# Optimization experiments

Hardware: AMD Instinct MI355X
Metric: run time of the kernel (lower is better)

Reference implementation:

```python
import jax, jax.numpy as jnp
import numpy as np

B, S, N, P = 16, 1, 6, 70000
H0, W0, DS = 448, 800, 4
H, W = H0 // DS, W0 // DS          # 112, 200
BEV_SIDE = 200


def _apply_4x4(RT, xyz):
    # RT: [M,4,4], xyz: [M,P,3] -> [M,P,3]
    xyz1 = jnp.concatenate([xyz, jnp.ones_like(xyz[..., :1])], axis=-1)
    return jnp.einsum('mij,mpj->mpi', RT, xyz1)[..., :3]


def _scale_intrinsics4(K, sx, sy):
    # K: [M,3,3] pinhole intrinsics -> scaled, embedded in 4x4
    M = K.shape[0]
    K4 = jnp.tile(jnp.eye(4, dtype=K.dtype), (M, 1, 1))
    K4 = K4.at[:, 0, 0].set(K[:, 0, 0] * sx)
    K4 = K4.at[:, 1, 1].set(K[:, 1, 1] * sy)
    K4 = K4.at[:, 0, 2].set(K[:, 0, 2] * sx)
    K4 = K4.at[:, 1, 2].set(K[:, 1, 2] * sy)
    return K4


def setup_inputs() -> dict:
    rng = np.random.default_rng(0)
    pts = rng.uniform(-50.0, 50.0, size=(B, 1, 1, P, 3)).astype(np.float32)
    pts[..., 2] = rng.uniform(-2.0, 4.0, size=(B, 1, 1, P)).astype(np.float32)
    ilu = rng.uniform(0.0, 255.0, size=(B, 1, 1, P, 1)).astype(np.float32)
    pcloud = np.concatenate([pts, ilu], axis=-1)
    # extrinsics: cam-to-car pose, 6 cameras at yaw 0..300deg
    E = np.tile(np.eye(4, dtype=np.float32), (B, S, N, 1, 1))
    for n in range(N):
        a = 2.0 * np.pi * n / N
        c, s = np.cos(a), np.sin(a)
        E[:, :, n, :3, :3] = np.array([[c, -s, 0], [s, c, 0], [0, 0, 1]], np.float32)
        E[:, :, n, :3, 3] = np.array([2.0 * c, 2.0 * s, 1.5], np.float32)
    K = np.tile(np.eye(3, dtype=np.float32), (B, S, N, 1, 1))
    K[..., 0, 0] = 500.0
    K[..., 1, 1] = 500.0
    K[..., 0, 2] = W0 / 2.0
    K[..., 1, 2] = H0 / 2.0
    V = np.tile(np.eye(4, dtype=np.float32), (B, 1, 1, 1, 1))
    V[..., 0, 0] = 2.0
    V[..., 1, 1] = 2.0
    V[..., 0, 3] = 100.0
    V[..., 1, 3] = 100.0
    return {
        'pcloud': jnp.asarray(pcloud),
        'extrinsics': jnp.asarray(E),
        'intrinsics': jnp.asarray(K),
        'view': jnp.asarray(V),
        'bev_side': BEV_SIDE,
    }


def reference(pcloud, extrinsics, intrinsics, view, bev_side):
    sx = sy = 1.0 / DS
    bsn = B * S * N
    lidar_coords = pcloud[:, 0, 0, :, :3]                      # [B,P,3]
    ilu = jnp.repeat(pcloud[:, 0, 0, :, 3], N, axis=0)         # [BSN,P]
    view2 = view[:, 0, 0]                                      # [B,4,4]
    lidar_view = _apply_4x4(jnp.linalg.inv(view2), lidar_coords)
    xyz_car = jnp.repeat(lidar_view, N, axis=0)                # [BSN,P,3]
    K = intrinsics.reshape(bsn, 3, 3)
    E = extrinsics.reshape(bsn, 4, 4)
    Rt = jnp.swapaxes(E[:, :3, :3], 1, 2)
    Einv = E.at[:, :3, :3].set(Rt).at[:, :3, 3:4].set(-jnp.matmul(Rt, E[:, :3, 3:4]))
    pixel_from_car = jnp.matmul(_scale_intrinsics4(K, sx, sy), Einv)
    z = _apply_4x4(Einv, xyz_car)[:, :, 2]                     # cam-frame depth
    xyz_pixel = _apply_4x4(pixel_from_car, xyz_car)            # [BSN,P,3]
    normalizer = xyz_pixel[:, :, 2]
    xy = xyz_pixel[:, :, :2] / jnp.maximum(normalizer[..., None], 1e-6)
    x_, y_ = xy[:, :, 0], xy[:, :, 1]
    valid = ((x_ > -0.5) & (x_ < W - 0.5) & (y_ > -0.5) & (y_ < H - 0.5) & (z > 0.0)).astype(pcloud.dtype)
    depth = jnp.clip(normalizer, 0.0, bev_side / 2 - 1) * valid
    vilu = jnp.clip(ilu * valid, 0.0, 255.0)
    ym = jnp.clip(y_, 0.0, H - 1).astype(jnp.int32)
    xm = jnp.clip(x_, 0.0, W - 1).astype(jnp.int32)
    b = jnp.broadcast_to(jnp.arange(bsn)[:, None], (bsn, P))
    depth_grid = jnp.zeros((bsn, H, W), pcloud.dtype).at[b, ym, xm].set(depth)
    ilu_grid = jnp.zeros((bsn, H, W), pcloud.dtype).at[b, ym, xm].set(vilu)
    ilu_grid = jnp.log1p(ilu_grid) / np.log(256.0)
    depth_grid = depth_grid / (bev_side / 2)
    return jnp.concatenate([depth_grid[:, None], ilu_grid[:, None]], axis=1)  # [BSN,2,H,W]
```

## Files before the change

kernel.cpp:

```cpp
#include <hip/hip_runtime.h>
#include <math.h>

#define B_    16
#define N_    6
#define P_    70000
#define H_    112
#define W_    200
#define HW_   (H_ * W_)
#define BSN_  (B_ * N_)
#define QROWS  28
#define QCELLS (QROWS * W_)
#define NSLAB  4
#define THREADS_ 1024

#define NBUCKET (BSN_ * NSLAB)
#define ARENA_U32 ((size_t)NBUCKET * P_)
#define WS_NEED ((ARENA_U32 + 2 * NBUCKET) * 4)

#define CC0 0
#define CC1 199
#define CC2 28416
#define CC3 28615


__device__ __forceinline__ float rdot(const float r[4], float x, float y, float z) {
    float s = r[0] * x;
    s = fmaf(r[1], y, s);
    s = fmaf(r[2], z, s);
    return s + r[3];
}

__device__ __forceinline__ float rdot4(float r0, float r1, float r2, float r3,
                                       float x, float y, float z) {
    float s = r0 * x;
    s = fmaf(r1, y, s);
    s = fmaf(r2, z, s);
    return s + r3;
}

__device__ __forceinline__ void inv4(const float* m, float* o) {
    float inv[16];
    inv[0]  =  m[5]*m[10]*m[15] - m[5]*m[11]*m[14] - m[9]*m[6]*m[15] + m[9]*m[7]*m[14] + m[13]*m[6]*m[11] - m[13]*m[7]*m[10];
    inv[4]  = -m[4]*m[10]*m[15] + m[4]*m[11]*m[14] + m[8]*m[6]*m[15] - m[8]*m[7]*m[14] - m[12]*m[6]*m[11] + m[12]*m[7]*m[10];
    inv[8]  =  m[4]*m[9]*m[15]  - m[4]*m[11]*m[13] - m[8]*m[5]*m[15] + m[8]*m[7]*m[13] + m[12]*m[5]*m[11] - m[12]*m[7]*m[9];
    inv[12] = -m[4]*m[9]*m[14]  + m[4]*m[10]*m[13] + m[8]*m[5]*m[14] - m[8]*m[6]*m[13] - m[12]*m[5]*m[10] + m[12]*m[6]*m[9];
    inv[1]  = -m[1]*m[10]*m[15] + m[1]*m[11]*m[14] + m[9]*m[2]*m[15] - m[9]*m[3]*m[14] - m[13]*m[2]*m[11] + m[13]*m[3]*m[10];
    inv[5]  =  m[0]*m[10]*m[15] - m[0]*m[11]*m[14] - m[8]*m[2]*m[15] + m[8]*m[3]*m[14] + m[12]*m[2]*m[11] - m[12]*m[3]*m[10];
    inv[9]  = -m[0]*m[9]*m[15]  + m[0]*m[11]*m[13] + m[8]*m[1]*m[15] - m[8]*m[3]*m[13] - m[12]*m[1]*m[11] + m[12]*m[3]*m[9];
    inv[13] =  m[0]*m[9]*m[14]  - m[0]*m[10]*m[13] - m[8]*m[1]*m[14] + m[8]*m[2]*m[13] + m[12]*m[1]*m[10] - m[12]*m[2]*m[9];
    inv[2]  =  m[1]*m[6]*m[15]  - m[1]*m[7]*m[14]  - m[5]*m[2]*m[15] + m[5]*m[3]*m[14] + m[13]*m[2]*m[7]  - m[13]*m[3]*m[6];
    inv[6]  = -m[0]*m[6]*m[15]  + m[0]*m[7]*m[14]  + m[4]*m[2]*m[15] - m[4]*m[3]*m[14] - m[12]*m[2]*m[7]  + m[12]*m[3]*m[6];
    inv[10] =  m[0]*m[5]*m[15]  - m[0]*m[7]*m[13]  - m[4]*m[1]*m[15] + m[4]*m[3]*m[13] + m[12]*m[1]*m[7]  - m[12]*m[3]*m[5];
    inv[14] = -m[0]*m[5]*m[14]  + m[0]*m[6]*m[13]  + m[4]*m[1]*m[14] - m[4]*m[2]*m[13] - m[12]*m[1]*m[6]  + m[12]*m[2]*m[5];
    inv[3]  = -m[1]*m[6]*m[11]  + m[1]*m[7]*m[10]  + m[5]*m[2]*m[11] - m[5]*m[3]*m[10] - m[9]*m[2]*m[7]   + m[9]*m[3]*m[6];
    inv[7]  =  m[0]*m[6]*m[11]  - m[0]*m[7]*m[10]  - m[4]*m[2]*m[11] + m[4]*m[3]*m[10] + m[8]*m[2]*m[7]   - m[8]*m[3]*m[6];
    inv[11] = -m[0]*m[5]*m[11]  + m[0]*m[7]*m[9]   + m[4]*m[1]*m[11] - m[4]*m[3]*m[9]  - m[8]*m[1]*m[7]   + m[8]*m[3]*m[5];
    inv[15] =  m[0]*m[5]*m[10]  - m[0]*m[6]*m[9]   - m[4]*m[1]*m[10] + m[4]*m[2]*m[9]  + m[8]*m[1]*m[6]   - m[8]*m[2]*m[5];
    float det = m[0]*inv[0] + m[1]*inv[4] + m[2]*inv[8] + m[3]*inv[12];
    float rdet = 1.0f / det;
    for (int i = 0; i < 16; ++i) o[i] = inv[i] * rdet;
}

__device__ __forceinline__ void cam_mats(const float* Ein, const float* Kin,
                                         float E2[4], float PFC[3][4]) {
    float Einv[4][4];
    for (int i = 0; i < 3; ++i)
        for (int j = 0; j < 3; ++j)
            Einv[i][j] = Ein[j * 4 + i];
    for (int i = 0; i < 3; ++i) {
        float s = Ein[0 * 4 + i] * Ein[0 * 4 + 3];
        s = fmaf(Ein[1 * 4 + i], Ein[1 * 4 + 3], s);
        s = fmaf(Ein[2 * 4 + i], Ein[2 * 4 + 3], s);
        Einv[i][3] = -s;
    }
    Einv[3][0] = Ein[12]; Einv[3][1] = Ein[13];
    Einv[3][2] = Ein[14]; Einv[3][3] = Ein[15];

    float K4[4][4] = {};
    K4[0][0] = Kin[0] * 0.25f;  K4[0][2] = Kin[2] * 0.25f;
    K4[1][1] = Kin[4] * 0.25f;  K4[1][2] = Kin[5] * 0.25f;
    K4[2][2] = 1.0f;            K4[3][3] = 1.0f;

    for (int i = 0; i < 3; ++i)
        for (int j = 0; j < 4; ++j) {
            float s = K4[i][0] * Einv[0][j];
            s = fmaf(K4[i][1], Einv[1][j], s);
            s = fmaf(K4[i][2], Einv[2][j], s);
            s = fmaf(K4[i][3], Einv[3][j], s);
            PFC[i][j] = s;
        }
    for (int j = 0; j < 4; ++j) E2[j] = Einv[2][j];
}


__global__ __launch_bounds__(2 * NBUCKET) void k_init_meta(int* __restrict__ meta) {
    const int t = threadIdx.x;
    meta[t] = (t < NBUCKET) ? 0 : -1;
}


#define K1CH 69

__global__ __launch_bounds__(THREADS_) void k_bucket2(
        const float4* __restrict__ pc, const float* __restrict__ extr,
        const float* __restrict__ intr, const float* __restrict__ view,
        unsigned int* __restrict__ arena, int* __restrict__ cursors,
        int* __restrict__ gcorner) {
    __shared__ float sM[84];
    __shared__ int   cnt[16][24];
    __shared__ int   wbase[16][24];
    __shared__ int   gb[24];
    __shared__ int   lc[24];

    const int b    = blockIdx.x;
    const int t    = threadIdx.x;
    const int lane = t & 63;
    const int w    = t >> 6;

    if (t == 0) {
        float Vi[16];
        inv4(&view[b * 16], Vi);
        for (int k = 0; k < 12; ++k) sM[k] = Vi[k];
    } else if (t >= 64 && t < 64 + N_) {
        int n = t - 64;
        float E2[4], PFC[3][4];
        cam_mats(&extr[(b * N_ + n) * 16], &intr[(b * N_ + n) * 9], E2, PFC);
        for (int i = 0; i < 3; ++i)
            for (int j = 0; j < 4; ++j) sM[12 + n * 12 + i * 4 + j] = PFC[i][j];
    }
    if (t >= 128 && t < 152) lc[t - 128] = -1;
    __syncthreads();

    const int p = blockIdx.y * THREADS_ + t;
    const bool valid = (p < P_);
    float4 pt = make_float4(0.f, 0.f, 0.f, 0.f);
    if (valid) pt = pc[(size_t)b * P_ + p];
    float lx = rdot(&sM[0], pt.x, pt.y, pt.z);
    float ly = rdot(&sM[4], pt.x, pt.y, pt.z);
    float lz = rdot(&sM[8], pt.x, pt.y, pt.z);

    const unsigned long long lt = (1ull << lane) - 1ull;
    const int pwbase = blockIdx.y * THREADS_ + w * 64;
    int stash[6];

    #pragma unroll
    for (int n = 0; n < 6; ++n) {
        const float* Pm = &sM[12 + n * 12];
        float px = rdot(&Pm[0], lx, ly, lz);
        float py = rdot(&Pm[4], lx, ly, lz);
        float pz = rdot(&Pm[8], lx, ly, lz);
        float denom = fmaxf(pz, 1e-6f);
        float x_ = px / denom;
        float y_ = py / denom;
        int ym = (int)fminf(fmaxf(y_, 0.0f), (float)(H_ - 1));
        int xm = (int)fminf(fmaxf(x_, 0.0f), (float)(W_ - 1));
        int code = (ym << 8) | xm;
        bool is_c = (code == CC0) | (code == CC1) | (code == CC2) | (code == CC3);
        unsigned long long m0 = __ballot(valid && code == CC0);
        unsigned long long m1 = __ballot(valid && code == CC1);
        unsigned long long m2 = __ballot(valid && code == CC2);
        unsigned long long m3 = __ballot(valid && code == CC3);
        if (lane == 0) {
            if (m0) atomicMax(&lc[n * 4 + 0], pwbase + 63 - __builtin_clzll(m0));
            if (m1) atomicMax(&lc[n * 4 + 1], pwbase + 63 - __builtin_clzll(m1));
            if (m2) atomicMax(&lc[n * 4 + 2], pwbase + 63 - __builtin_clzll(m2));
            if (m3) atomicMax(&lc[n * 4 + 3], pwbase + 63 - __builtin_clzll(m3));
        }
        bool act = valid && !is_c;
        int slab = (ym * 585) >> 14;
        unsigned long long ACT = __ballot(act);
        unsigned long long B0  = __ballot(act && (slab & 1));
        unsigned long long B1  = __ballot(act && (slab & 2));
        unsigned long long mm  = ((slab & 1) ? B0 : ~B0) &
                                 ((slab & 2) ? B1 : ~B1) & ACT;
        int rank = (int)__popcll(mm & lt);
        if (lane < 4) {
            unsigned long long ml = ((lane & 1) ? B0 : ~B0) &
                                    ((lane & 2) ? B1 : ~B1) & ACT;
            cnt[w][n * 4 + lane] = (int)__popcll(ml);
        }
        stash[n] = act ? ((code << 9) | (rank << 3) | slab) : -1;
    }
    __syncthreads();

    if (t < 24) {
        int s = 0;
        for (int w2 = 0; w2 < 16; ++w2) { wbase[w2][t] = s; s += cnt[w2][t]; }
        gb[t] = atomicAdd(&cursors[b * 24 + t], s);
    }
    __syncthreads();

    #pragma unroll
    for (int n = 0; n < 6; ++n) {
        int sv = stash[n];
        if (sv >= 0) {
            int slab = sv & 7;
            int rank = (sv >> 3) & 63;
            int code = sv >> 9;
            int j    = n * 4 + slab;
            size_t slot = (size_t)((b * N_ + n) * NSLAB + slab) * P_ +
                          (size_t)(gb[j] + wbase[w][j] + rank);
            arena[slot] = ((unsigned int)code << 17) | (unsigned int)p;
        }
    }
    if (t < 24 && lc[t] >= 0) atomicMax(&gcorner[b * 24 + t], lc[t]);
}


__global__ __launch_bounds__(THREADS_) void k_scatfin3(
        const float4* __restrict__ pc, const unsigned int* __restrict__ arena,
        const int* __restrict__ cursors, const int* __restrict__ gcorner,
        const float* __restrict__ extr, const float* __restrict__ intr,
        const float* __restrict__ view,
        float* __restrict__ out, const int* __restrict__ bev_side_p) {
    __shared__ int   win[QCELLS];
    __shared__ float sM[28];

    const int i   = blockIdx.x;
    const int xcd = i & 7;
    const int j   = i >> 3;
    const int b   = xcd + 8 * (j >= 24 ? 1 : 0);
    const int r   = j % 24;
    const int cam = r >> 2;
    const int q   = r & 3;
    const int m   = b * N_ + cam;
    const int rlo = q * QROWS;
    const int t   = threadIdx.x;

    if (t == 0) {
        float Vi[16];
        inv4(&view[b * 16], Vi);
        for (int k = 0; k < 12; ++k) sM[k] = Vi[k];
    } else if (t == 64) {
        float E2[4], PFC[3][4];
        cam_mats(&extr[m * 16], &intr[m * 9], E2, PFC);
        for (int ii = 0; ii < 3; ++ii)
            for (int jj = 0; jj < 4; ++jj) sM[12 + ii * 4 + jj] = PFC[ii][jj];
        for (int jj = 0; jj < 4; ++jj) sM[24 + jj] = E2[jj];
    }
    for (int k = t; k < QCELLS; k += THREADS_) win[k] = -1;
    __syncthreads();

    if (t == 0) {
        if (q == 0) {
            int g0 = gcorner[m * 4 + 0], g1 = gcorner[m * 4 + 1];
            if (g0 >= 0) atomicMax(&win[0],   g0);
            if (g1 >= 0) atomicMax(&win[199], g1);
        } else if (q == 3) {
            int g2 = gcorner[m * 4 + 2], g3 = gcorner[m * 4 + 3];
            if (g2 >= 0) atomicMax(&win[(H_ - 1 - rlo) * W_ + 0],   g2);
            if (g3 >= 0) atomicMax(&win[(H_ - 1 - rlo) * W_ + 199], g3);
        }
    }

    const unsigned int* seg = arena + (size_t)(m * NSLAB + q) * P_;
    const int cntq = cursors[b * 24 + cam * 4 + q];
    const int nv = cntq >> 2;
    const uint4* seg4 = (const uint4*)seg;
    for (int v = t; v < nv; v += THREADS_) {
        uint4 e4 = seg4[v];
        unsigned int es[4] = {e4.x, e4.y, e4.z, e4.w};
        #pragma unroll
        for (int h = 0; h < 4; ++h) {
            unsigned int e = es[h];
            int code = (int)(e >> 17);
            int p    = (int)(e & 0x1FFFFu);
            atomicMax(&win[((code >> 8) - rlo) * W_ + (code & 255)], p);
        }
    }
    {
        int k2 = (nv << 2) + t;
        if (k2 < cntq) {
            unsigned int e = seg[k2];
            int code = (int)(e >> 17);
            int p    = (int)(e & 0x1FFFFu);
            atomicMax(&win[((code >> 8) - rlo) * W_ + (code & 255)], p);
        }
    }
    __syncthreads();

    const float bev_half = (float)bev_side_p[0] * 0.5f;
    const float clip_hi  = bev_half - 1.0f;
    const float4* pcb = pc + (size_t)b * P_;
    const int base0 = (m * 2) * HW_ + rlo * W_;
    for (int rr = t; rr < QCELLS; rr += THREADS_) {
        int wv = win[rr];
        float depth = 0.0f, iluv = 0.0f;
        if (wv >= 0) {
            float4 pt = pcb[wv];
            float lx = rdot4(sM[0],  sM[1],  sM[2],  sM[3],  pt.x, pt.y, pt.z);
            float ly = rdot4(sM[4],  sM[5],  sM[6],  sM[7],  pt.x, pt.y, pt.z);
            float lz = rdot4(sM[8],  sM[9],  sM[10], sM[11], pt.x, pt.y, pt.z);
            float z  = rdot4(sM[24], sM[25], sM[26], sM[27], lx, ly, lz);
            float px = rdot4(sM[12], sM[13], sM[14], sM[15], lx, ly, lz);
            float py = rdot4(sM[16], sM[17], sM[18], sM[19], lx, ly, lz);
            float pz = rdot4(sM[20], sM[21], sM[22], sM[23], lx, ly, lz);
            float denom = fmaxf(pz, 1e-6f);
            float x_ = px / denom;
            float y_ = py / denom;
            bool valid = (x_ > -0.5f) && (x_ < (float)W_ - 0.5f) &&
                         (y_ > -0.5f) && (y_ < (float)H_ - 0.5f) && (z > 0.0f);
            if (valid) {
                float d = fminf(fmaxf(pz, 0.0f), clip_hi);
                depth = d / bev_half;
                float vi = fminf(fmaxf(pt.w, 0.0f), 255.0f);
                iluv = log1pf(vi) / 5.545177444479562f;
            }
        }
        out[base0 + rr]       = depth;
        out[base0 + HW_ + rr] = iluv;
    }
}


#define HALF_ 56
#define CELLS_ (HALF_ * W_)
#define PMAIN 69632
#define PTAIL (P_ - PMAIN)

__global__ __launch_bounds__(THREADS_, 4) void k_lidar_ilp(
        const float4* __restrict__ pc, const float* __restrict__ extr,
        const float* __restrict__ intr, const float* __restrict__ view,
        float* __restrict__ out, const int* __restrict__ bev_side_p) {
    __shared__ int   win[CELLS_];
    __shared__ float sM[28];

    const int i    = blockIdx.x;
    const int xcd  = i & 7;
    const int s    = i >> 3;
    const int b    = xcd + 8 * (s >= 12 ? 1 : 0);
    const int c12  = s % 12;
    const int m    = b * N_ + (c12 >> 1);
    const int rlo  = (c12 & 1) * HALF_;
    const int t    = threadIdx.x;

    if (t == 0) {
        float Vi[16];
        inv4(&view[b * 16], Vi);
        for (int k = 0; k < 12; ++k) sM[k] = Vi[k];
    } else if (t == 64) {
        float E2[4], PFC[3][4];
        cam_mats(&extr[m * 16], &intr[m * 9], E2, PFC);
        for (int ii = 0; ii < 3; ++ii)
            for (int jj = 0; jj < 4; ++jj) sM[12 + ii * 4 + jj] = PFC[ii][jj];
        for (int jj = 0; jj < 4; ++jj) sM[24 + jj] = E2[jj];
    }
    for (int k = t; k < CELLS_; k += THREADS_) win[k] = -1;
    __syncthreads();

    const float V0 = sM[0],  V1 = sM[1],  V2 = sM[2],  V3 = sM[3];
    const float V4 = sM[4],  V5 = sM[5],  V6 = sM[6],  V7 = sM[7];
    const float V8 = sM[8],  V9 = sM[9],  V10 = sM[10], V11 = sM[11];
    const float P00 = sM[12], P01 = sM[13], P02 = sM[14], P03 = sM[15];
    const float P10 = sM[16], P11 = sM[17], P12 = sM[18], P13 = sM[19];
    const float P20 = sM[20], P21 = sM[21], P22 = sM[22], P23 = sM[23];

    const float4* pcb = pc + (size_t)b * P_;
    int c0 = -1, c1 = -1, c2 = -1, c3 = -1;

#define PROC(PT, PIDX)                                                        \
    {                                                                         \
        float lx = rdot4(V0, V1, V2,  V3,  (PT).x, (PT).y, (PT).z);           \
        float ly = rdot4(V4, V5, V6,  V7,  (PT).x, (PT).y, (PT).z);           \
        float lz = rdot4(V8, V9, V10, V11, (PT).x, (PT).y, (PT).z);           \
        float px = rdot4(P00, P01, P02, P03, lx, ly, lz);                     \
        float py = rdot4(P10, P11, P12, P13, lx, ly, lz);                     \
        float pz = rdot4(P20, P21, P22, P23, lx, ly, lz);                     \
        float denom = fmaxf(pz, 1e-6f);                                       \
        float x_ = px / denom;                                                \
        float y_ = py / denom;                                                \
        int ym = (int)fminf(fmaxf(y_, 0.0f), (float)(H_ - 1));                \
        int xm = (int)fminf(fmaxf(x_, 0.0f), (float)(W_ - 1));                \
        bool is_c = (xm == 0 || xm == W_ - 1) && (ym == 0 || ym == H_ - 1);   \
        int code = ((ym != 0) << 1) | (xm != 0);                              \
        c0 = (is_c && code == 0) ? (PIDX) : c0;                               \
        c1 = (is_c && code == 1) ? (PIDX) : c1;                               \
        c2 = (is_c && code == 2) ? (PIDX) : c2;                               \
        c3 = (is_c && code == 3) ? (PIDX) : c3;                               \
        int rr = ym - rlo;                                                    \
        if (!is_c && (unsigned)rr < (unsigned)HALF_)                          \
            atomicMax(&win[rr * W_ + xm], (PIDX));                            \
    }

    for (int base = 0; base < PMAIN; base += 4 * THREADS_) {
        float4 q0 = pcb[base + t];
        float4 q1 = pcb[base + t + THREADS_];
        float4 q2 = pcb[base + t + 2 * THREADS_];
        float4 q3 = pcb[base + t + 3 * THREADS_];
        PROC(q0, base + t)
        PROC(q1, base + t + THREADS_)
        PROC(q2, base + t + 2 * THREADS_)
        PROC(q3, base + t + 3 * THREADS_)
    }
    if (t < PTAIL) {
        float4 q = pcb[PMAIN + t];
        PROC(q, PMAIN + t)
    }
#undef PROC

    for (int d = 32; d; d >>= 1) {
        c0 = max(c0, __shfl_xor(c0, d));
        c1 = max(c1, __shfl_xor(c1, d));
        c2 = max(c2, __shfl_xor(c2, d));
        c3 = max(c3, __shfl_xor(c3, d));
    }
    if ((t & 63) == 0) {
        if (rlo == 0) {
            if (c0 >= 0) atomicMax(&win[0],   c0);
            if (c1 >= 0) atomicMax(&win[199], c1);
        } else {
            if (c2 >= 0) atomicMax(&win[(H_ - 1 - rlo) * W_ + 0],   c2);
            if (c3 >= 0) atomicMax(&win[(H_ - 1 - rlo) * W_ + 199], c3);
        }
    }
    __syncthreads();

    const float bev_half = (float)bev_side_p[0] * 0.5f;
    const float clip_hi  = bev_half - 1.0f;
    const float E20 = sM[24], E21 = sM[25], E22 = sM[26], E23 = sM[27];
    const int base0 = (m * 2) * HW_ + rlo * W_;
    for (int r = t; r < CELLS_; r += THREADS_) {
        int w = win[r];
        float depth = 0.0f, iluv = 0.0f;
        if (w >= 0) {
            float4 pt = pcb[w];
            float lx = rdot4(V0, V1, V2,  V3,  pt.x, pt.y, pt.z);
            float ly = rdot4(V4, V5, V6,  V7,  pt.x, pt.y, pt.z);
            float lz = rdot4(V8, V9, V10, V11, pt.x, pt.y, pt.z);
            float z  = rdot4(E20, E21, E22, E23, lx, ly, lz);
            float px = rdot4(P00, P01, P02, P03, lx, ly, lz);
            float py = rdot4(P10, P11, P12, P13, lx, ly, lz);
            float pz = rdot4(P20, P21, P22, P23, lx, ly, lz);
            float denom = fmaxf(pz, 1e-6f);
            float x_ = px / denom;
            float y_ = py / denom;
            bool valid = (x_ > -0.5f) && (x_ < (float)W_ - 0.5f) &&
                         (y_ > -0.5f) && (y_ < (float)H_ - 0.5f) && (z > 0.0f);
            if (valid) {
                float d = fminf(fmaxf(pz, 0.0f), clip_hi);
                depth = d / bev_half;
                float vi = fminf(fmaxf(pt.w, 0.0f), 255.0f);
                iluv = log1pf(vi) / 5.545177444479562f;
            }
        }
        out[base0 + r]       = depth;
        out[base0 + HW_ + r] = iluv;
    }
}


extern "C" void kernel_launch(void* const* d_in, const int* in_sizes, int n_in,
                              void* d_out, int out_size, void* d_ws, size_t ws_size,
                              hipStream_t stream) {
    const float4* pc  = (const float4*)d_in[0];
    const float* extr = (const float*)d_in[1];
    const float* intr = (const float*)d_in[2];
    const float* view = (const float*)d_in[3];
    const int*   bev  = (const int*)d_in[4];
    float* out = (float*)d_out;

    if (ws_size >= WS_NEED) {
        unsigned int* arena = (unsigned int*)d_ws;
        int* cursors = (int*)(arena + ARENA_U32);
        int* gcorner = cursors + NBUCKET;
        k_init_meta<<<dim3(1), dim3(2 * NBUCKET), 0, stream>>>(cursors);
        k_bucket2<<<dim3(B_, K1CH), dim3(THREADS_), 0, stream>>>(
            pc, extr, intr, view, arena, cursors, gcorner);
        k_scatfin3<<<dim3(NBUCKET), dim3(THREADS_), 0, stream>>>(
            pc, arena, cursors, gcorner, extr, intr, view, out, bev);
    } else {
        k_lidar_ilp<<<dim3(BSN_ * 2), dim3(THREADS_), 0, stream>>>(
            pc, extr, intr, view, out, bev);
    }
}
```

Before: 52.94 us.

## Move corner-cell handling into scatter kernel and shrink bucket blocks

The bucketing kernel no longer special-cases the four clamped corner cells with extra ballots and shared/global atomicMax. Corner points are now bucketed normally and resolved in the scatter kernel through per-thread max plus a wave shuffle reduction. This drops the gcorner buffer and its initialization. The bucketing block size also drops from 1024 to 256 threads with four times as many blocks, giving cheaper per-block prefix sums and more parallelism, at the cost of more global cursor atomics. The slab multiplier changes from 585 to 586, and the scatter kernel adds a row-range guard for entries outside the block's rows.

```diff
diff --git a/kernel.cpp b/kernel.cpp
--- a/kernel.cpp
+++ b/kernel.cpp
@@ -11,11 +11,13 @@
 #define QROWS  28
 #define QCELLS (QROWS * W_)
 #define NSLAB  4
-#define THREADS_ 1024
+#define T2_   1024
+#define T1_   256
+#define K1CH  274
 
 #define NBUCKET (BSN_ * NSLAB)
 #define ARENA_U32 ((size_t)NBUCKET * P_)
-#define WS_NEED ((ARENA_U32 + 2 * NBUCKET) * 4)
+#define WS_NEED ((ARENA_U32 + NBUCKET) * 4)
 
 #define CC0 0
 #define CC1 199
@@ -93,24 +95,19 @@
 }
 
 
-__global__ __launch_bounds__(2 * NBUCKET) void k_init_meta(int* __restrict__ meta) {
-    const int t = threadIdx.x;
-    meta[t] = (t < NBUCKET) ? 0 : -1;
-}
-
-
-#define K1CH 69
-
-__global__ __launch_bounds__(THREADS_) void k_bucket2(
+__global__ __launch_bounds__(NBUCKET) void k_init_cur(int* __restrict__ cursors) {
+    cursors[threadIdx.x] = 0;
+}
+
+
+__global__ __launch_bounds__(T1_) void k_bucket4(
         const float4* __restrict__ pc, const float* __restrict__ extr,
         const float* __restrict__ intr, const float* __restrict__ view,
-        unsigned int* __restrict__ arena, int* __restrict__ cursors,
-        int* __restrict__ gcorner) {
+        unsigned int* __restrict__ arena, int* __restrict__ cursors) {
     __shared__ float sM[84];
-    __shared__ int   cnt[16][24];
-    __shared__ int   wbase[16][24];
+    __shared__ int   cnt[4][24];
+    __shared__ int   wbase[4][24];
     __shared__ int   gb[24];
-    __shared__ int   lc[24];
 
     const int b    = blockIdx.x;
     const int t    = threadIdx.x;
@@ -128,10 +125,9 @@
         for (int i = 0; i < 3; ++i)
             for (int j = 0; j < 4; ++j) sM[12 + n * 12 + i * 4 + j] = PFC[i][j];
     }
-    if (t >= 128 && t < 152) lc[t - 128] = -1;
-    __syncthreads();
-
-    const int p = blockIdx.y * THREADS_ + t;
+    __syncthreads();
+
+    const int p = blockIdx.y * T1_ + t;
     const bool valid = (p < P_);
     float4 pt = make_float4(0.f, 0.f, 0.f, 0.f);
     if (valid) pt = pc[(size_t)b * P_ + p];
@@ -139,8 +135,8 @@
     float ly = rdot(&sM[4], pt.x, pt.y, pt.z);
     float lz = rdot(&sM[8], pt.x, pt.y, pt.z);
 
-    const unsigned long long lt = (1ull << lane) - 1ull;
-    const int pwbase = blockIdx.y * THREADS_ + w * 64;
+    const unsigned long long lt  = (1ull << lane) - 1ull;
+    const unsigned long long ACT = __ballot(valid);
     int stash[6];
 
     #pragma unroll
@@ -155,61 +151,48 @@
         int ym = (int)fminf(fmaxf(y_, 0.0f), (float)(H_ - 1));
         int xm = (int)fminf(fmaxf(x_, 0.0f), (float)(W_ - 1));
         int code = (ym << 8) | xm;
-        bool is_c = (code == CC0) | (code == CC1) | (code == CC2) | (code == CC3);
-        unsigned long long m0 = __ballot(valid && code == CC0);
-        unsigned long long m1 = __ballot(valid && code == CC1);
-        unsigned long long m2 = __ballot(valid && code == CC2);
-        unsigned long long m3 = __ballot(valid && code == CC3);
-        if (lane == 0) {
-            if (m0) atomicMax(&lc[n * 4 + 0], pwbase + 63 - __builtin_clzll(m0));
-            if (m1) atomicMax(&lc[n * 4 + 1], pwbase + 63 - __builtin_clzll(m1));
-            if (m2) atomicMax(&lc[n * 4 + 2], pwbase + 63 - __builtin_clzll(m2));
-            if (m3) atomicMax(&lc[n * 4 + 3], pwbase + 63 - __builtin_clzll(m3));
-        }
-        bool act = valid && !is_c;
-        int slab = (ym * 585) >> 14;
-        unsigned long long ACT = __ballot(act);
-        unsigned long long B0  = __ballot(act && (slab & 1));
-        unsigned long long B1  = __ballot(act && (slab & 2));
-        unsigned long long mm  = ((slab & 1) ? B0 : ~B0) &
-                                 ((slab & 2) ? B1 : ~B1) & ACT;
+        int slab = (ym * 586) >> 14;
+        unsigned long long B0 = __ballot(valid && (slab & 1));
+        unsigned long long B1 = __ballot(valid && (slab & 2));
+        unsigned long long mm = ((slab & 1) ? B0 : ~B0) &
+                                ((slab & 2) ? B1 : ~B1) & ACT;
         int rank = (int)__popcll(mm & lt);
         if (lane < 4) {
             unsigned long long ml = ((lane & 1) ? B0 : ~B0) &
                                     ((lane & 2) ? B1 : ~B1) & ACT;
             cnt[w][n * 4 + lane] = (int)__popcll(ml);
         }
-        stash[n] = act ? ((code << 9) | (rank << 3) | slab) : -1;
+        stash[n] = (code << 9) | (rank << 3) | slab;
     }
     __syncthreads();
 
     if (t < 24) {
         int s = 0;
-        for (int w2 = 0; w2 < 16; ++w2) { wbase[w2][t] = s; s += cnt[w2][t]; }
+        #pragma unroll
+        for (int w2 = 0; w2 < 4; ++w2) { wbase[w2][t] = s; s += cnt[w2][t]; }
         gb[t] = atomicAdd(&cursors[b * 24 + t], s);
     }
     __syncthreads();
 
-    #pragma unroll
-    for (int n = 0; n < 6; ++n) {
-        int sv = stash[n];
-        if (sv >= 0) {
+    if (valid) {
+        #pragma unroll
+        for (int n = 0; n < 6; ++n) {
+            int sv   = stash[n];
             int slab = sv & 7;
             int rank = (sv >> 3) & 63;
             int code = sv >> 9;
             int j    = n * 4 + slab;
-            size_t slot = (size_t)((b * N_ + n) * NSLAB + slab) * P_ +
+            size_t slot = (size_t)(b * 24 + j) * P_ +
                           (size_t)(gb[j] + wbase[w][j] + rank);
             arena[slot] = ((unsigned int)code << 17) | (unsigned int)p;
         }
     }
-    if (t < 24 && lc[t] >= 0) atomicMax(&gcorner[b * 24 + t], lc[t]);
-}
-
-
-__global__ __launch_bounds__(THREADS_) void k_scatfin3(
+}
+
+
+__global__ __launch_bounds__(T2_) void k_scatfin4(
         const float4* __restrict__ pc, const unsigned int* __restrict__ arena,
-        const int* __restrict__ cursors, const int* __restrict__ gcorner,
+        const int* __restrict__ cursors,
         const float* __restrict__ extr, const float* __restrict__ intr,
         const float* __restrict__ view,
         float* __restrict__ out, const int* __restrict__ bev_side_p) {
@@ -238,26 +221,18 @@
             for (int jj = 0; jj < 4; ++jj) sM[12 + ii * 4 + jj] = PFC[ii][jj];
         for (int jj = 0; jj < 4; ++jj) sM[24 + jj] = E2[jj];
     }
-    for (int k = t; k < QCELLS; k += THREADS_) win[k] = -1;
-    __syncthreads();
-
-    if (t == 0) {
-        if (q == 0) {
-            int g0 = gcorner[m * 4 + 0], g1 = gcorner[m * 4 + 1];
-            if (g0 >= 0) atomicMax(&win[0],   g0);
-            if (g1 >= 0) atomicMax(&win[199], g1);
-        } else if (q == 3) {
-            int g2 = gcorner[m * 4 + 2], g3 = gcorner[m * 4 + 3];
-            if (g2 >= 0) atomicMax(&win[(H_ - 1 - rlo) * W_ + 0],   g2);
-            if (g3 >= 0) atomicMax(&win[(H_ - 1 - rlo) * W_ + 199], g3);
-        }
-    }
-
-    const unsigned int* seg = arena + (size_t)(m * NSLAB + q) * P_;
+    for (int k = t; k < QCELLS; k += T2_) win[k] = -1;
+    __syncthreads();
+
+    const unsigned int* seg = arena + (size_t)(b * 24 + cam * 4 + q) * P_;
     const int cntq = cursors[b * 24 + cam * 4 + q];
+    const int ccA = (q == 0) ? CC0 : ((q == 3) ? CC2 : -1);
+    const int ccB = (q == 0) ? CC1 : ((q == 3) ? CC3 : -1);
+    int cA = -1, cB = -1;
+
     const int nv = cntq >> 2;
     const uint4* seg4 = (const uint4*)seg;
-    for (int v = t; v < nv; v += THREADS_) {
+    for (int v = t; v < nv; v += T2_) {
         uint4 e4 = seg4[v];
         unsigned int es[4] = {e4.x, e4.y, e4.z, e4.w};
         #pragma unroll
@@ -265,7 +240,13 @@
             unsigned int e = es[h];
             int code = (int)(e >> 17);
             int p    = (int)(e & 0x1FFFFu);
-            atomicMax(&win[((code >> 8) - rlo) * W_ + (code & 255)], p);
+            if (code == ccA)      cA = max(cA, p);
+            else if (code == ccB) cB = max(cB, p);
+            else {
+                int rr = (code >> 8) - rlo;
+                if ((unsigned)rr < (unsigned)QROWS)
+                    atomicMax(&win[rr * W_ + (code & 255)], p);
+            }
         }
     }
     {
@@ -274,7 +255,26 @@
             unsigned int e = seg[k2];
             int code = (int)(e >> 17);
             int p    = (int)(e & 0x1FFFFu);
-            atomicMax(&win[((code >> 8) - rlo) * W_ + (code & 255)], p);
+            if (code == ccA)      cA = max(cA, p);
+            else if (code == ccB) cB = max(cB, p);
+            else {
+                int rr = (code >> 8) - rlo;
+                if ((unsigned)rr < (unsigned)QROWS)
+                    atomicMax(&win[rr * W_ + (code & 255)], p);
+            }
+        }
+    }
+    for (int d = 32; d; d >>= 1) {
+        cA = max(cA, __shfl_xor(cA, d));
+        cB = max(cB, __shfl_xor(cB, d));
+    }
+    if ((t & 63) == 0) {
+        if (q == 0) {
+            if (cA >= 0) atomicMax(&win[0],   cA);
+            if (cB >= 0) atomicMax(&win[199], cB);
+        } else if (q == 3) {
+            if (cA >= 0) atomicMax(&win[(H_ - 1 - rlo) * W_ + 0],   cA);
+            if (cB >= 0) atomicMax(&win[(H_ - 1 - rlo) * W_ + 199], cB);
         }
     }
     __syncthreads();
@@ -283,7 +283,7 @@
     const float clip_hi  = bev_half - 1.0f;
     const float4* pcb = pc + (size_t)b * P_;
     const int base0 = (m * 2) * HW_ + rlo * W_;
-    for (int rr = t; rr < QCELLS; rr += THREADS_) {
+    for (int rr = t; rr < QCELLS; rr += T2_) {
         int wv = win[rr];
         float depth = 0.0f, iluv = 0.0f;
         if (wv >= 0) {
@@ -318,7 +318,7 @@
 #define PMAIN 69632
 #define PTAIL (P_ - PMAIN)
 
-__global__ __launch_bounds__(THREADS_, 4) void k_lidar_ilp(
+__global__ __launch_bounds__(T2_, 4) void k_lidar_ilp(
         const float4* __restrict__ pc, const float* __restrict__ extr,
         const float* __restrict__ intr, const float* __restrict__ view,
         float* __restrict__ out, const int* __restrict__ bev_side_p) {
@@ -345,7 +345,7 @@
             for (int jj = 0; jj < 4; ++jj) sM[12 + ii * 4 + jj] = PFC[ii][jj];
         for (int jj = 0; jj < 4; ++jj) sM[24 + jj] = E2[jj];
     }
-    for (int k = t; k < CELLS_; k += THREADS_) win[k] = -1;
+    for (int k = t; k < CELLS_; k += T2_) win[k] = -1;
     __syncthreads();
 
     const float V0 = sM[0],  V1 = sM[1],  V2 = sM[2],  V3 = sM[3];
@@ -382,15 +382,15 @@
             atomicMax(&win[rr * W_ + xm], (PIDX));                            \
     }
 
-    for (int base = 0; base < PMAIN; base += 4 * THREADS_) {
+    for (int base = 0; base < PMAIN; base += 4 * T2_) {
         float4 q0 = pcb[base + t];
-        float4 q1 = pcb[base + t + THREADS_];
-        float4 q2 = pcb[base + t + 2 * THREADS_];
-        float4 q3 = pcb[base + t + 3 * THREADS_];
+        float4 q1 = pcb[base + t + T2_];
+        float4 q2 = pcb[base + t + 2 * T2_];
+        float4 q3 = pcb[base + t + 3 * T2_];
         PROC(q0, base + t)
-        PROC(q1, base + t + THREADS_)
-        PROC(q2, base + t + 2 * THREADS_)
-        PROC(q3, base + t + 3 * THREADS_)
+        PROC(q1, base + t + T2_)
+        PROC(q2, base + t + 2 * T2_)
+        PROC(q3, base + t + 3 * T2_)
     }
     if (t < PTAIL) {
         float4 q = pcb[PMAIN + t];
@@ -419,7 +419,7 @@
     const float clip_hi  = bev_half - 1.0f;
     const float E20 = sM[24], E21 = sM[25], E22 = sM[26], E23 = sM[27];
     const int base0 = (m * 2) * HW_ + rlo * W_;
-    for (int r = t; r < CELLS_; r += THREADS_) {
+    for (int r = t; r < CELLS_; r += T2_) {
         int w = win[r];
         float depth = 0.0f, iluv = 0.0f;
         if (w >= 0) {
@@ -462,14 +462,13 @@
     if (ws_size >= WS_NEED) {
         unsigned int* arena = (unsigned int*)d_ws;
         int* cursors = (int*)(arena + ARENA_U32);
-        int* gcorner = cursors + NBUCKET;
-        k_init_meta<<<dim3(1), dim3(2 * NBUCKET), 0, stream>>>(cursors);
-        k_bucket2<<<dim3(B_, K1CH), dim3(THREADS_), 0, stream>>>(
-            pc, extr, intr, view, arena, cursors, gcorner);
-        k_scatfin3<<<dim3(NBUCKET), dim3(THREADS_), 0, stream>>>(
-            pc, arena, cursors, gcorner, extr, intr, view, out, bev);
+        k_init_cur<<<dim3(1), dim3(NBUCKET), 0, stream>>>(cursors);
+        k_bucket4<<<dim3(B_, K1CH), dim3(T1_), 0, stream>>>(
+            pc, extr, intr, view, arena, cursors);
+        k_scatfin4<<<dim3(NBUCKET), dim3(T2_), 0, stream>>>(
+            pc, arena, cursors, extr, intr, view, out, bev);
     } else {
-        k_lidar_ilp<<<dim3(BSN_ * 2), dim3(THREADS_), 0, stream>>>(
+        k_lidar_ilp<<<dim3(BSN_ * 2), dim3(T2_), 0, stream>>>(
             pc, extr, intr, view, out, bev);
     }
 }
```

New measurement: 50.05 us. -5.5%, faster.
